# Kernel optimization log

Measured on AMD Instinct MI355X. Metric: run time of the kernel, lower is better.

Reference implementation:

```python
import jax, jax.numpy as jnp
import numpy as np

# ---- config (matches init_kwargs) ----
B, NP, DIM, HEADS, DH, NDIM = 32, 576, 512, 8, 64, 16
N = NP + 1                 # seq len incl cls token = 577
INNER = HEADS * DH         # 512


def setup_inputs() -> dict:
    key = jax.random.key(0)
    ks = jax.random.split(key, 11)
    D2 = 2 * DIM  # bidirectional EMA doubles kernel dim
    return {
        "x": jax.random.normal(ks[0], (B, N, DIM), jnp.float32),
        "W_qk": jax.random.normal(ks[1], (DIM, 2 * INNER), jnp.float32) / np.float32(np.sqrt(DIM)),
        "W_v": jax.random.normal(ks[2], (DIM, INNER), jnp.float32) / np.float32(np.sqrt(DIM)),
        "W_out": jax.random.normal(ks[3], (INNER, DIM), jnp.float32) / np.float32(np.sqrt(INNER)),
        "b_out": jnp.zeros((DIM,), jnp.float32),
        "rel_bias": jax.random.normal(ks[4], (2 * N - 1,), jnp.float32) * 0.02,
        "ema_delta": jax.random.normal(ks[5], (D2, NDIM, 1), jnp.float32),
        "ema_alpha": jax.random.normal(ks[6], (D2, NDIM, 1), jnp.float32),
        "ema_beta": jax.random.normal(ks[7], (D2, NDIM, 1), jnp.float32) * 0.5,
        "ema_gamma": jax.random.normal(ks[8], (D2, NDIM), jnp.float32) * 0.5,
        "ema_omega": jax.random.normal(ks[9], (DIM,), jnp.float32),
    }


def _ema_move(x, delta, alpha, beta, gamma, omega):
    """Bidirectional MultiHeadEMA (MEGA) via FFT convolution. x: (B, L, D)."""
    b, L, d = x.shape
    scale = jnp.asarray(np.sqrt(1.0 / NDIM), x.dtype)
    p = jax.nn.sigmoid(delta)                      # (2D, N, 1)
    q = 1.0 - p * jax.nn.sigmoid(alpha)            # (2D, N, 1), in (0,1)
    vander = jnp.arange(L, dtype=x.dtype)[None, None, :] * jnp.log(q)  # (2D, N, L)
    kern = (p * beta) * jnp.exp(vander)            # (2D, N, L)
    k = jnp.einsum('dnl,dn->dl', kern, gamma * scale)  # (2D, L)
    k1, k2 = k[:d], k[d:]
    # combined bidirectional kernel, length 2L-1
    kk = jnp.pad(k1, ((0, 0), (L - 1, 0))) + jnp.pad(k2[:, ::-1], ((0, 0), (0, L - 1)))
    xt = jnp.pad(x.transpose(0, 2, 1), ((0, 0), (0, 0), (L - 1, 0)))  # (B, D, 2L-1)
    fft_len = 2 * L - 1
    nfft = 2 * fft_len
    out = jnp.fft.irfft(jnp.fft.rfft(xt, n=nfft) * jnp.fft.rfft(kk, n=nfft)[None], n=nfft)
    s = 2 * L - 2
    out = out[..., s:s + L].transpose(0, 2, 1).astype(x.dtype)  # (B, L, D)
    return jax.nn.silu(out + x * omega)


def _rel_pos_bias(rb, seq_len):
    """RelativePositionalBias (MEGA): (2*N-1,) param -> (seq_len, seq_len) bias."""
    max_pos = N
    bvec = rb[max_pos - seq_len: max_pos + seq_len - 1]   # (2*seq_len-1,)
    t = jnp.pad(bvec, (0, seq_len))
    t = jnp.tile(t, seq_len)[:-seq_len].reshape(seq_len, 3 * seq_len - 2)
    r = (2 * seq_len - 1) // 2
    return t[:, r:t.shape[1] - r]


def reference(x, W_qk, W_v, W_out, b_out, rel_bias,
              ema_delta, ema_alpha, ema_beta, ema_gamma, ema_omega):
    b, n, _ = x.shape
    cls_tok = x[:, :1]
    moved = _ema_move(x[:, 1:], ema_delta, ema_alpha, ema_beta, ema_gamma, ema_omega)
    xm = jnp.concatenate([cls_tok, moved], axis=1)        # (B, N, DIM)
    q, k = jnp.split(xm @ W_qk, 2, axis=-1)
    v = xm @ W_v                                          # smooth_v_as_well=True

    def heads(t):
        return t.reshape(b, n, HEADS, DH).transpose(0, 2, 1, 3)  # (B, H, N, DH)

    q, k, v = heads(q), heads(k), heads(v)
    dots = jnp.einsum('bhid,bhjd->bhij', q, k) * (DH ** -0.5)
    attn = jax.nn.softmax(dots, axis=-1)
    attn = attn + _rel_pos_bias(rel_bias, n)[None, None]  # bias added AFTER softmax
    out = jnp.einsum('bhij,bhjd->bhid', attn, v)
    out = out.transpose(0, 2, 1, 3).reshape(b, n, INNER)
    return out @ W_out + b_out
```

## Files before the change

### kernel.cpp

```cpp
#include <hip/hip_runtime.h>

typedef unsigned short ushort;

typedef __bf16 bf16x8 __attribute__((ext_vector_type(8)));
typedef float  f32x4  __attribute__((ext_vector_type(4)));
typedef float  f32x2  __attribute__((ext_vector_type(2)));
typedef unsigned short u16x8 __attribute__((ext_vector_type(8)));
typedef unsigned short u16x4 __attribute__((ext_vector_type(4)));
typedef unsigned int   u32x2 __attribute__((ext_vector_type(2)));

static constexpr int BB   = 32;
static constexpr int NN   = 577;
static constexpr int LL   = 576;
static constexpr int DIMC = 512;
static constexpr int BN   = BB * NN;

static constexpr size_t SZ_WQKVT = 1536ull * 512 * 2;
static constexpr size_t SZ_WOUTT = 512ull * 512 * 2;
static constexpr size_t SZ_QK    = (size_t)BN * 1024 * 2;
static constexpr size_t SZ_V     = (size_t)BN * 512 * 2;
static constexpr size_t SZ_VT    = 256ull * 64 * 640 * 2;
static constexpr size_t OFF_WQKVT = 0;
static constexpr size_t OFF_WOUTT = OFF_WQKVT + SZ_WQKVT;
static constexpr size_t OFF_QTAB  = OFF_WOUTT + SZ_WOUTT;
static constexpr size_t OFF_CTAB  = OFF_QTAB + 65536;
static constexpr size_t OFF_QK    = OFF_CTAB + 65536;
static constexpr size_t OFF_V     = OFF_QK + SZ_QK;
static constexpr size_t OFF_REGION= OFF_V + SZ_V;
static constexpr size_t OFF_XM    = OFF_REGION;
static constexpr size_t OFF_VT    = OFF_REGION;
static constexpr size_t OFF_AO    = OFF_REGION + SZ_VT;
static constexpr size_t OFF_ST    = OFF_AO;
static constexpr size_t WS_NEEDED = OFF_AO + SZ_V;

__device__ __forceinline__ ushort bf16bits(float f) {
  unsigned int u = __builtin_bit_cast(unsigned int, f);
  u = (u + 0x7fffu + ((u >> 16) & 1u)) >> 16;
  return (ushort)u;
}
__device__ __forceinline__ unsigned int bf16pk(float lo, float hi) {
  unsigned int u0 = __builtin_bit_cast(unsigned int, lo);
  unsigned int u1 = __builtin_bit_cast(unsigned int, hi);
  unsigned int a0 = u0 + 0x7fffu + ((u0 >> 16) & 1u);
  unsigned int a1 = u1 + 0x7fffu + ((u1 >> 16) & 1u);
  return __builtin_amdgcn_perm(a1, a0, 0x07060302);
}
__device__ __forceinline__ float sigmoidf_(float z) { return 1.f / (1.f + __expf(-z)); }
__device__ __forceinline__ float siluf(float z)     { return z / (1.f + __expf(-z)); }
__device__ __forceinline__ void gload16(const ushort* g, ushort* l) {
  __builtin_amdgcn_global_load_lds(
      (const __attribute__((address_space(1))) unsigned int*)g,
      (__attribute__((address_space(3))) unsigned int*)l, 16, 0, 0);
}

__global__ __launch_bounds__(256) void k_prep(
    const float* __restrict__ delta, const float* __restrict__ alpha,
    const float* __restrict__ beta,  const float* __restrict__ gamma,
    const float* __restrict__ Wqk,   const float* __restrict__ Wv,
    const float* __restrict__ Wout,
    float* __restrict__ qtab, float* __restrict__ ctab,
    ushort* __restrict__ Wqkvt, ushort* __restrict__ Woutt)
{
  int idx = blockIdx.x * 256 + threadIdx.x;
  if (idx < 16384) {
    float p = sigmoidf_(delta[idx]);
    float q = 1.f - p * sigmoidf_(alpha[idx]);
    qtab[idx] = q;
    ctab[idx] = p * beta[idx] * gamma[idx] * 0.25f;
  }
  int i2 = idx - 16384;
  if (i2 >= 0 && i2 < 1536 * 512) {
    int n = i2 >> 9, k = i2 & 511;
    float w = (n < 1024) ? Wqk[k * 1024 + n] : Wv[k * 512 + (n - 1024)];
    Wqkvt[i2] = bf16bits(w);
  }
  int i3 = i2 - 1536 * 512;
  if (i3 >= 0 && i3 < 512 * 512) {
    int n = i3 >> 9, k = i3 & 511;
    Woutt[i3] = bf16bits(Wout[k * 512 + n]);
  }
}


__global__ __launch_bounds__(64) void k_ema_p1(
    const float* __restrict__ x, const float* __restrict__ qtab,
    float* __restrict__ st)
{
  const int gx = blockIdx.x, cy = blockIdx.y, b = blockIdx.z;
  if (gx < 8) {
    const int d = gx * 64 + threadIdx.x;
    f32x2 q[8], h[8];
    #pragma unroll
    for (int n = 0; n < 8; ++n) {
      q[n] = *(const f32x2*)(qtab + d * 16 + 2 * n);
      h[n] = (f32x2){0.f, 0.f};
    }
    const float* xp = x + ((size_t)b * NN + 1) * DIMC + d;
    const int blo = cy * 9;
    float xn[8];
    #pragma unroll
    for (int u = 0; u < 8; ++u) xn[u] = xp[(blo * 8 + u) * DIMC];
    for (int blk = blo; blk < blo + 9; ++blk) {
      float xv[8];
      #pragma unroll
      for (int u = 0; u < 8; ++u) xv[u] = xn[u];
      if (blk < blo + 8) {
        #pragma unroll
        for (int u = 0; u < 8; ++u) xn[u] = xp[((blk + 1) * 8 + u) * DIMC];
      }
      #pragma unroll
      for (int u = 0; u < 8; ++u) {
        f32x2 x2 = {xv[u], xv[u]};
        #pragma unroll
        for (int n = 0; n < 8; ++n) h[n] = __builtin_elementwise_fma(q[n], h[n], x2);
      }
    }
    float* sp = st + (((size_t)b * 8 + cy) * 16) * 512 + d;
    #pragma unroll
    for (int n = 0; n < 8; ++n) { sp[(2*n) * 512] = h[n][0]; sp[(2*n+1) * 512] = h[n][1]; }
  } else {
    const int d = (gx - 8) * 64 + threadIdx.x;
    f32x2 q[8], g[8];
    #pragma unroll
    for (int n = 0; n < 8; ++n) {
      q[n] = *(const f32x2*)(qtab + (d + 512) * 16 + 2 * n);
      g[n] = (f32x2){0.f, 0.f};
    }
    const float* xp = x + ((size_t)b * NN + 1) * DIMC + d;
    const int blo = (7 - cy) * 9;
    float xn[8];
    #pragma unroll
    for (int u = 0; u < 8; ++u) xn[u] = xp[((blo + 8) * 8 + u) * DIMC];
    for (int blk = blo + 8; blk >= blo; --blk) {
      float xv[8];
      #pragma unroll
      for (int u = 0; u < 8; ++u) xv[u] = xn[u];
      if (blk > blo) {
        #pragma unroll
        for (int u = 0; u < 8; ++u) xn[u] = xp[((blk - 1) * 8 + u) * DIMC];
      }
      #pragma unroll
      for (int u = 7; u >= 0; --u) {
        f32x2 x2 = {xv[u], xv[u]};
        #pragma unroll
        for (int n = 0; n < 8; ++n) g[n] = __builtin_elementwise_fma(q[n], g[n], x2);
      }
    }
    float* sp = st + (((size_t)(32 + b) * 8 + cy) * 16) * 512 + d;
    #pragma unroll
    for (int n = 0; n < 8; ++n) { sp[(2*n) * 512] = g[n][0]; sp[(2*n+1) * 512] = g[n][1]; }
  }
}

__global__ __launch_bounds__(256) void k_ema_mid(
    const float* __restrict__ qtab, float* __restrict__ st)
{
  int idx = blockIdx.x * 256 + threadIdx.x;
  int d = idx & 511;
  int rest = idx >> 9;
  int n = rest & 15;
  int db = rest >> 4;
  int dir = db >> 5;
  float q = qtab[(((size_t)dir << 9) + d) * 16 + n];
  float q2 = q * q, q4 = q2 * q2, q8 = q4 * q4;
  float q16 = q8 * q8, q32 = q16 * q16, q64 = q32 * q32;
  float qL = q64 * q8;
  float h = 0.f;
  float* sp = st + ((size_t)db * 128 + n) * 512 + d;
  #pragma unroll
  for (int c = 0; c < 8; ++c) {
    float tmp = (c < 7) ? sp[c * 8192] : 0.f;
    sp[c * 8192] = h;
    h = fmaf(qL, h, tmp);
  }
}

__global__ __launch_bounds__(64) void k_ema_fuse(
    const float* __restrict__ x, const float* __restrict__ qtab,
    const float* __restrict__ ctab, const float* __restrict__ st,
    const float* __restrict__ omega, ushort* __restrict__ xm)
{
  __shared__ _Float16 yb[72 * 64];
  const int lane = threadIdx.x;
  const int gx = blockIdx.x, cy = blockIdx.y, b = blockIdx.z;
  const int d = gx * 64 + lane;
  const float* xp = x + ((size_t)b * NN + 1 + cy * 72) * DIMC + d;
  {
    f32x2 q[8], c[8], g[8];
    const float* sp = st + (((size_t)(32 + b) * 8 + (7 - cy)) * 16) * 512 + d;
    #pragma unroll
    for (int n = 0; n < 8; ++n) {
      q[n] = *(const f32x2*)(qtab + (d + 512) * 16 + 2 * n);
      c[n] = *(const f32x2*)(ctab + (d + 512) * 16 + 2 * n);
      g[n] = (f32x2){sp[(2*n) * 512], sp[(2*n+1) * 512]};
    }
    float xn[8];
    #pragma unroll
    for (int u = 0; u < 8; ++u) xn[u] = xp[(64 + u) * DIMC];
    for (int blk = 8; blk >= 0; --blk) {
      float xv[8];
      #pragma unroll
      for (int u = 0; u < 8; ++u) xv[u] = xn[u];
      if (blk > 0) {
        #pragma unroll
        for (int u = 0; u < 8; ++u) xn[u] = xp[((blk - 1) * 8 + u) * DIMC];
      }
      #pragma unroll
      for (int u = 7; u >= 0; --u) {
        f32x2 x2 = {xv[u], xv[u]};
        f32x2 yv = {0.f, 0.f};
        #pragma unroll
        for (int n = 0; n < 8; ++n) {
          g[n] = __builtin_elementwise_fma(q[n], g[n], x2);
          yv   = __builtin_elementwise_fma(c[n], g[n], yv);
        }
        yb[(blk * 8 + u) * 64 + lane] = (_Float16)(yv[0] + yv[1]);
      }
    }
  }
  __syncthreads();
  {
    f32x2 q[8], c[8], h[8];
    const float* sp = st + (((size_t)b * 8 + cy) * 16) * 512 + d;
    #pragma unroll
    for (int n = 0; n < 8; ++n) {
      q[n] = *(const f32x2*)(qtab + d * 16 + 2 * n);
      c[n] = *(const f32x2*)(ctab + d * 16 + 2 * n);
      h[n] = (f32x2){sp[(2*n) * 512], sp[(2*n+1) * 512]};
    }
    const float om = omega[d];
    ushort* op = xm + ((size_t)b * NN + 1 + cy * 72) * DIMC + d;
    float xn[8];
    #pragma unroll
    for (int u = 0; u < 8; ++u) xn[u] = xp[u * DIMC];
    for (int blk = 0; blk < 9; ++blk) {
      float xv[8];
      #pragma unroll
      for (int u = 0; u < 8; ++u) xv[u] = xn[u];
      if (blk < 8) {
        #pragma unroll
        for (int u = 0; u < 8; ++u) xn[u] = xp[((blk + 1) * 8 + u) * DIMC];
      }
      #pragma unroll
      for (int u = 0; u < 8; ++u) {
        f32x2 x2 = {xv[u], xv[u]};
        f32x2 yv = {0.f, 0.f};
        #pragma unroll
        for (int n = 0; n < 8; ++n) {
          h[n] = __builtin_elementwise_fma(q[n], h[n], x2);
          yv   = __builtin_elementwise_fma(c[n], h[n], yv);
        }
        float s = (yv[0] + yv[1]) + (float)yb[(blk * 8 + u) * 64 + lane] + xv[u] * om;
        op[(blk * 8 + u) * DIMC] = bf16bits(siluf(s));
      }
    }
  }
  if (cy == 0) {
    size_t e0 = ((size_t)b * NN) * DIMC + d;
    xm[e0] = bf16bits(x[e0]);
  }
}

__global__ __launch_bounds__(256) void k_qkv(
    const ushort* __restrict__ A, const ushort* __restrict__ Bt,
    ushort* __restrict__ qk, ushort* __restrict__ v)
{
  __shared__ alignas(16) ushort lA[128 * 32];
  __shared__ alignas(16) ushort lB[128 * 32];
  const int tid = threadIdx.x, wv = tid >> 6, lane = tid & 63;
  const int quad = lane >> 4, c16 = lane & 15;
  const int fid = blockIdx.y * 12 + blockIdx.x;
  const int xcd = fid & 7, ord = fid >> 3;
  const int wg  = (xcd < 4 ? xcd * 218 : 872 + (xcd - 4) * 217) + ord;
  const int row0 = (wg / 12) * 128, n0 = (wg % 12) * 128;
  const int wm = (wv >> 1) * 64, wn = (wv & 1) * 64;
  const int sr  = wv * 32 + (lane >> 2);
  const int scs = ((lane & 3) ^ (sr & 3)) * 8;
  int ga[2], gb[2];
  #pragma unroll
  for (int s = 0; s < 2; ++s) {
    int r = row0 + sr + s * 16; if (r > BN - 1) r = BN - 1;
    ga[s] = r;
    gb[s] = n0 + sr + s * 16;
  }
  const int xread = (quad ^ (c16 & 3)) * 8;
  f32x4 z4 = {0.f, 0.f, 0.f, 0.f};
  f32x4 acc[4][4];
  #pragma unroll
  for (int mi = 0; mi < 4; ++mi)
    #pragma unroll
    for (int ni = 0; ni < 4; ++ni) acc[mi][ni] = z4;

  for (int kt = 0; kt < 16; ++kt) {
    const int k0 = kt * 32;
    __syncthreads();
    #pragma unroll
    for (int s = 0; s < 2; ++s) {
      gload16(A  + (size_t)ga[s] * 512 + k0 + scs, lA + (wv * 32 + s * 16) * 32);
      gload16(Bt + (size_t)gb[s] * 512 + k0 + scs, lB + (wv * 32 + s * 16) * 32);
    }
    __syncthreads();
    bf16x8 af[4], bfv[4];
    #pragma unroll
    for (int mi = 0; mi < 4; ++mi)
      af[mi] = *(const bf16x8*)(lA + (wm + mi * 16 + c16) * 32 + xread);
    #pragma unroll
    for (int ni = 0; ni < 4; ++ni)
      bfv[ni] = *(const bf16x8*)(lB + (wn + ni * 16 + c16) * 32 + xread);
    #pragma unroll
    for (int mi = 0; mi < 4; ++mi)
      #pragma unroll
      for (int ni = 0; ni < 4; ++ni)
        acc[mi][ni] = __builtin_amdgcn_mfma_f32_16x16x32_bf16(af[mi], bfv[ni], acc[mi][ni], 0, 0, 0);
  }
  const bool isv = (n0 >= 1024);
  const float osc = (n0 < 512) ? 0.1803368801111f : 1.0f;
  #pragma unroll
  for (int mi = 0; mi < 4; ++mi) {
    #pragma unroll
    for (int r = 0; r < 4; ++r) {
      int grow = row0 + wm + mi * 16 + quad * 4 + r;
      if (grow < BN) {
        #pragma unroll
        for (int ni = 0; ni < 4; ++ni) {
          int col = n0 + wn + ni * 16 + c16;
          ushort vb = bf16bits(acc[mi][ni][r] * osc);
          if (!isv) qk[(size_t)grow * 1024 + col] = vb;
          else      v[(size_t)grow * 512 + (col - 1024)] = vb;
        }
      }
    }
  }
}

__global__ __launch_bounds__(256) void k_vtrans(
    const ushort* __restrict__ v, ushort* __restrict__ vt)
{
  __shared__ alignas(16) ushort lt[64 * 72];
  const int tid = threadIdx.x;
  const int bh = blockIdx.y, b = bh >> 3, h = bh & 7;
  const int j0 = blockIdx.x * 64;
  #pragma unroll
  for (int pass = 0; pass < 2; ++pass) {
    int cch = pass * 256 + tid;
    int jl = cch >> 3, cc = cch & 7;
    int gj = j0 + jl;
    u16x8 val = {0, 0, 0, 0, 0, 0, 0, 0};
    if (gj < 577) val = *(const u16x8*)(v + ((size_t)(b * NN + gj)) * 512 + h * 64 + cc * 8);
    *(u16x8*)(lt + jl * 72 + cc * 8) = val;
  }
  __syncthreads();
  #pragma unroll
  for (int pass = 0; pass < 2; ++pass) {
    int cch = pass * 256 + tid;
    int dh = cch >> 3, jc = cch & 7;
    u16x8 o;
    #pragma unroll
    for (int e = 0; e < 8; ++e) o[e] = lt[(jc * 8 + e) * 72 + dh];
    *(u16x8*)(vt + ((size_t)(bh * 64 + dh)) * 640 + j0 + jc * 8) = o;
  }
}

__global__ __launch_bounds__(256) void k_fattn(
    const ushort* __restrict__ qk, const ushort* __restrict__ vt,
    const float* __restrict__ relb, ushort* __restrict__ ao)
{
  __shared__ alignas(16) ushort lk[64 * 64];
  __shared__ alignas(16) ushort lv[64 * 64];
  __shared__ alignas(16) ushort lp[64 * 64];
  __shared__ ushort lbias16[1280];
  const int tid = threadIdx.x, wv = tid >> 6, lane = tid & 63;
  const int quad = lane >> 4, c16 = lane & 15;
  const int bh = blockIdx.x, b = bh >> 3, h = bh & 7;
  const int i0 = blockIdx.y * 64, wm = wv * 16;
  for (int t = tid; t < 1280; t += 256) {
    int idx = t - 64;
    lbias16[t] = (idx >= 0 && idx < 1153) ? bf16bits(relb[idx]) : (ushort)0;
  }
  bf16x8 aq[2];
  {
    int gi = i0 + wm + c16; if (gi > 576) gi = 576;
    const ushort* qp = qk + ((size_t)(b * NN + gi)) * 1024 + h * 64;
    #pragma unroll
    for (int kk = 0; kk < 2; ++kk)
      aq[kk] = *(const bf16x8*)(qp + (kk * 4 + quad) * 8);
  }
  const int s_r = tid >> 3, s_c = tid & 7;
  const ushort* kbase = qk + ((size_t)b * NN) * 1024 + 512 + h * 64 + s_c * 8;
  const ushort* vbase = vt + ((size_t)bh * 64) * 640 + s_c * 8;

  float lsum = 0.f;
  f32x4 z4 = {0.f, 0.f, 0.f, 0.f};
  f32x4 accp[4], accb[4];
  #pragma unroll
  for (int ns = 0; ns < 4; ++ns) { accp[ns] = z4; accb[ns] = z4; }

  u16x8 sk[2], sv[2];
  #pragma unroll
  for (int it = 0; it < 2; ++it) {
    int r = it * 32 + s_r;
    sk[it] = *(const u16x8*)(kbase + (size_t)r * 1024);
    sv[it] = *(const u16x8*)(vbase + (size_t)r * 640);
  }

  for (int jt = 0; jt < 10; ++jt) {
    __syncthreads();
    #pragma unroll
    for (int it = 0; it < 2; ++it) {
      int r = it * 32 + s_r;
      int pc = (s_c ^ (r & 7)) * 8;
      *(u16x8*)(lk + r * 64 + pc) = sk[it];
      *(u16x8*)(lv + r * 64 + pc) = sv[it];
    }
    __syncthreads();
    if (jt < 9) {
      const int j0n = (jt + 1) * 64;
      #pragma unroll
      for (int it = 0; it < 2; ++it) {
        int r = it * 32 + s_r;
        int gj = j0n + r; if (gj > 576) gj = 576;
        sk[it] = *(const u16x8*)(kbase + (size_t)gj * 1024);
        sv[it] = *(const u16x8*)(vbase + (size_t)r * 640 + j0n);
      }
    }
    f32x4 dacc[4] = {z4, z4, z4, z4};
    #pragma unroll
    for (int kk = 0; kk < 2; ++kk) {
      const int ck = kk * 4 + quad;
      #pragma unroll
      for (int ns = 0; ns < 4; ++ns) {
        const int row = ns * 16 + c16;
        bf16x8 bk = *(const bf16x8*)(lk + row * 64 + ((ck ^ (row & 7)) * 8));
        dacc[ns] = __builtin_amdgcn_mfma_f32_16x16x32_bf16(bk, aq[kk], dacc[ns], 0, 0, 0);
      }
    }
    {
      const int irow = wm + c16;
      const int xr = irow & 7;
      #pragma unroll
      for (int ns = 0; ns < 4; ++ns) {
        float ex[4];
        #pragma unroll
        for (int r = 0; r < 4; ++r) {
          float e = __builtin_amdgcn_exp2f(dacc[ns][r]);
          if (jt == 9 && (ns * 16 + quad * 4 + r) >= 1) e = 0.f;
          ex[r] = e;
        }
        lsum += (ex[0] + ex[1]) + (ex[2] + ex[3]);
        u32x2 pw = { bf16pk(ex[0], ex[1]), bf16pk(ex[2], ex[3]) };
        const int lc = ns * 2 + (quad >> 1);
        *(u32x2*)(lp + irow * 64 + ((lc ^ xr) * 8) + (quad & 1) * 4) = pw;
      }
    }
    const int j0 = jt * 64;
    #pragma unroll
    for (int kk = 0; kk < 2; ++kk) {
      const int ck = kk * 4 + quad;
      const int row = wm + c16;
      bf16x8 ap = *(const bf16x8*)(lp + row * 64 + ((ck ^ (row & 7)) * 8));
      u16x8 abu;
      const int base = 64 + 576 + j0 + kk * 32 + quad * 8 - (i0 + row);
      #pragma unroll
      for (int e = 0; e < 8; ++e) abu[e] = lbias16[base + e];
      bf16x8 ab = __builtin_bit_cast(bf16x8, abu);
      #pragma unroll
      for (int ns = 0; ns < 4; ++ns) {
        const int vrow = ns * 16 + c16;
        bf16x8 bV = *(const bf16x8*)(lv + vrow * 64 + ((ck ^ (vrow & 7)) * 8));
        accp[ns] = __builtin_amdgcn_mfma_f32_16x16x32_bf16(ap, bV, accp[ns], 0, 0, 0);
        accb[ns] = __builtin_amdgcn_mfma_f32_16x16x32_bf16(ab, bV, accb[ns], 0, 0, 0);
      }
    }
  }
  float tot = lsum;
  tot += __shfl_xor(tot, 16);
  tot += __shfl_xor(tot, 32);
  #pragma unroll
  for (int r = 0; r < 4; ++r) {
    float li = 1.f / __shfl(tot, quad * 4 + r);
    int ii = i0 + wm + quad * 4 + r;
    if (ii < 577) {
      #pragma unroll
      for (int ns = 0; ns < 4; ++ns)
        ao[((size_t)(b * NN + ii)) * 512 + h * 64 + ns * 16 + c16] =
            bf16bits(accp[ns][r] * li + accb[ns][r]);
    }
  }
}

__global__ __launch_bounds__(256) void k_out(
    const ushort* __restrict__ A, const ushort* __restrict__ Bt,
    const float* __restrict__ bout, float* __restrict__ out)
{
  __shared__ alignas(16) ushort lA[128 * 32];
  __shared__ alignas(16) ushort lB[128 * 32];
  const int tid = threadIdx.x, wv = tid >> 6, lane = tid & 63;
  const int quad = lane >> 4, c16 = lane & 15;
  const int row0 = blockIdx.y * 128, n0 = blockIdx.x * 128;
  const int wm = (wv >> 1) * 64, wn = (wv & 1) * 64;
  const int sr  = wv * 32 + (lane >> 2);
  const int scs = ((lane & 3) ^ (sr & 3)) * 8;
  int ga[2], gb[2];
  #pragma unroll
  for (int s = 0; s < 2; ++s) {
    int r = row0 + sr + s * 16; if (r > BN - 1) r = BN - 1;
    ga[s] = r;
    gb[s] = n0 + sr + s * 16;
  }
  const int xread = (quad ^ (c16 & 3)) * 8;
  f32x4 z4 = {0.f, 0.f, 0.f, 0.f};
  f32x4 acc[4][4];
  #pragma unroll
  for (int mi = 0; mi < 4; ++mi)
    #pragma unroll
    for (int ni = 0; ni < 4; ++ni) acc[mi][ni] = z4;

  for (int kt = 0; kt < 16; ++kt) {
    const int k0 = kt * 32;
    __syncthreads();
    #pragma unroll
    for (int s = 0; s < 2; ++s) {
      gload16(A  + (size_t)ga[s] * 512 + k0 + scs, lA + (wv * 32 + s * 16) * 32);
      gload16(Bt + (size_t)gb[s] * 512 + k0 + scs, lB + (wv * 32 + s * 16) * 32);
    }
    __syncthreads();
    bf16x8 af[4], bfv[4];
    #pragma unroll
    for (int mi = 0; mi < 4; ++mi)
      af[mi] = *(const bf16x8*)(lA + (wm + mi * 16 + c16) * 32 + xread);
    #pragma unroll
    for (int ni = 0; ni < 4; ++ni)
      bfv[ni] = *(const bf16x8*)(lB + (wn + ni * 16 + c16) * 32 + xread);
    #pragma unroll
    for (int mi = 0; mi < 4; ++mi)
      #pragma unroll
      for (int ni = 0; ni < 4; ++ni)
        acc[mi][ni] = __builtin_amdgcn_mfma_f32_16x16x32_bf16(af[mi], bfv[ni], acc[mi][ni], 0, 0, 0);
  }
  #pragma unroll
  for (int mi = 0; mi < 4; ++mi) {
    #pragma unroll
    for (int r = 0; r < 4; ++r) {
      int grow = row0 + wm + mi * 16 + quad * 4 + r;
      if (grow < BN) {
        #pragma unroll
        for (int ni = 0; ni < 4; ++ni) {
          int col = n0 + wn + ni * 16 + c16;
          out[(size_t)grow * 512 + col] = acc[mi][ni][r] + bout[col];
        }
      }
    }
  }
}

extern "C" void kernel_launch(void* const* d_in, const int* in_sizes, int n_in,
                              void* d_out, int out_size, void* d_ws, size_t ws_size,
                              hipStream_t stream) {
  (void)in_sizes; (void)n_in; (void)out_size;
  if (ws_size < WS_NEEDED) return;
  const float* x    = (const float*)d_in[0];
  const float* Wqk  = (const float*)d_in[1];
  const float* Wv   = (const float*)d_in[2];
  const float* Wout = (const float*)d_in[3];
  const float* bout = (const float*)d_in[4];
  const float* relb = (const float*)d_in[5];
  const float* edel = (const float*)d_in[6];
  const float* ealp = (const float*)d_in[7];
  const float* ebet = (const float*)d_in[8];
  const float* egam = (const float*)d_in[9];
  const float* eome = (const float*)d_in[10];

  char* ws = (char*)d_ws;
  ushort* Wqkvt = (ushort*)(ws + OFF_WQKVT);
  ushort* Woutt = (ushort*)(ws + OFF_WOUTT);
  float*  qtab  = (float*)(ws + OFF_QTAB);
  float*  ctab  = (float*)(ws + OFF_CTAB);
  ushort* qkb   = (ushort*)(ws + OFF_QK);
  ushort* vb    = (ushort*)(ws + OFF_V);
  ushort* xm    = (ushort*)(ws + OFF_XM);
  ushort* vtb   = (ushort*)(ws + OFF_VT);
  ushort* aob   = (ushort*)(ws + OFF_AO);
  float*  stf   = (float*)(ws + OFF_ST);
  float*  outp  = (float*)d_out;

  k_prep<<<dim3(4160), dim3(256), 0, stream>>>(edel, ealp, ebet, egam, Wqk, Wv, Wout,
                                               qtab, ctab, Wqkvt, Woutt);
  k_ema_p1<<<dim3(16, 7, 32), dim3(64), 0, stream>>>(x, qtab, stf);
  k_ema_mid<<<dim3(2048), dim3(256), 0, stream>>>(qtab, stf);
  k_ema_fuse<<<dim3(8, 8, 32), dim3(64), 0, stream>>>(x, qtab, ctab, stf, eome, xm);
  k_qkv<<<dim3(12, 145), dim3(256), 0, stream>>>(xm, Wqkvt, qkb, vb);
  k_vtrans<<<dim3(10, 256), dim3(256), 0, stream>>>(vb, vtb);
  k_fattn<<<dim3(256, 10), dim3(256), 0, stream>>>(qkb, vtb, relb, aob);
  k_out<<<dim3(4, 145), dim3(256), 0, stream>>>(aob, Woutt, bout, outp);
}
```

Measured before the change: 307.6 us.

## Double-buffer K/V tiles with direct global-to-LDS loads and 128-row query tiles

The attention kernel now uses two LDS buffers for K and V. The next tile is loaded with gload16 (direct global-to-LDS copies) while the current one is computed, which removes one barrier per iteration and the register staging. Each block now handles 128 query rows (two 16-row sub-tiles per wave), so every K/V tile loaded is reused twice and the grid shrinks to half. In exchange it uses more LDS and registers and launches fewer blocks, which can lower occupancy. The last tile now pads 128 rows instead of 64.

Result: faster. 296.9 us (-3.5%).

```diff
diff --git a/kernel.cpp b/kernel.cpp
--- a/kernel.cpp
+++ b/kernel.cpp
@@ -365,77 +365,76 @@
     const ushort* __restrict__ qk, const ushort* __restrict__ vt,
     const float* __restrict__ relb, ushort* __restrict__ ao)
 {
-  __shared__ alignas(16) ushort lk[64 * 64];
-  __shared__ alignas(16) ushort lv[64 * 64];
-  __shared__ alignas(16) ushort lp[64 * 64];
+  __shared__ alignas(16) ushort lk0[64 * 64];
+  __shared__ alignas(16) ushort lk1[64 * 64];
+  __shared__ alignas(16) ushort lv0[64 * 64];
+  __shared__ alignas(16) ushort lv1[64 * 64];
+  __shared__ alignas(16) ushort lp[128 * 64];
   __shared__ ushort lbias16[1280];
   const int tid = threadIdx.x, wv = tid >> 6, lane = tid & 63;
   const int quad = lane >> 4, c16 = lane & 15;
   const int bh = blockIdx.x, b = bh >> 3, h = bh & 7;
-  const int i0 = blockIdx.y * 64, wm = wv * 16;
+  const int i0 = blockIdx.y * 128, wm = wv * 32;
   for (int t = tid; t < 1280; t += 256) {
     int idx = t - 64;
     lbias16[t] = (idx >= 0 && idx < 1153) ? bf16bits(relb[idx]) : (ushort)0;
   }
-  bf16x8 aq[2];
-  {
-    int gi = i0 + wm + c16; if (gi > 576) gi = 576;
+  bf16x8 aq[2][2];
+  #pragma unroll
+  for (int ms = 0; ms < 2; ++ms) {
+    int gi = i0 + wm + ms * 16 + c16; if (gi > 576) gi = 576;
     const ushort* qp = qk + ((size_t)(b * NN + gi)) * 1024 + h * 64;
     #pragma unroll
     for (int kk = 0; kk < 2; ++kk)
-      aq[kk] = *(const bf16x8*)(qp + (kk * 4 + quad) * 8);
-  }
-  const int s_r = tid >> 3, s_c = tid & 7;
-  const ushort* kbase = qk + ((size_t)b * NN) * 1024 + 512 + h * 64 + s_c * 8;
-  const ushort* vbase = vt + ((size_t)bh * 64) * 640 + s_c * 8;
-
-  float lsum = 0.f;
+      aq[ms][kk] = *(const bf16x8*)(qp + (kk * 4 + quad) * 8);
+  }
+  const int lr = lane >> 3, lc = lane & 7;
+  const ushort* kroot = qk + ((size_t)b * NN) * 1024 + 512 + h * 64;
+  const ushort* vroot = vt + ((size_t)bh * 64) * 640;
+
+  float lsum[2] = {0.f, 0.f};
   f32x4 z4 = {0.f, 0.f, 0.f, 0.f};
-  f32x4 accp[4], accb[4];
-  #pragma unroll
-  for (int ns = 0; ns < 4; ++ns) { accp[ns] = z4; accb[ns] = z4; }
-
-  u16x8 sk[2], sv[2];
-  #pragma unroll
-  for (int it = 0; it < 2; ++it) {
-    int r = it * 32 + s_r;
-    sk[it] = *(const u16x8*)(kbase + (size_t)r * 1024);
-    sv[it] = *(const u16x8*)(vbase + (size_t)r * 640);
-  }
+  f32x4 accp[2][4], accb[2][4];
+  #pragma unroll
+  for (int ms = 0; ms < 2; ++ms)
+    #pragma unroll
+    for (int ns = 0; ns < 4; ++ns) { accp[ms][ns] = z4; accb[ms][ns] = z4; }
+
+  #define STAGE_TILE(J0, DK, DV)                                              \
+    {                                                                         \
+      _Pragma("unroll")                                                       \
+      for (int s = 0; s < 2; ++s) {                                           \
+        const int r  = wv * 16 + s * 8 + lr;                                  \
+        const int sc = (lc ^ (r & 7)) * 8;                                    \
+        int gj = (J0) + r; if (gj > 576) gj = 576;                            \
+        gload16(kroot + (size_t)gj * 1024 + sc, (DK) + (wv * 16 + s * 8) * 64); \
+        gload16(vroot + (size_t)r * 640 + (J0) + sc, (DV) + (wv * 16 + s * 8) * 64); \
+      }                                                                       \
+    }
+
+  STAGE_TILE(0, lk0, lv0)
 
   for (int jt = 0; jt < 10; ++jt) {
+    const ushort* ck_ = (jt & 1) ? lk1 : lk0;
+    const ushort* cv_ = (jt & 1) ? lv1 : lv0;
+    ushort* nk_ = (jt & 1) ? lk0 : lk1;
+    ushort* nv_ = (jt & 1) ? lv0 : lv1;
     __syncthreads();
-    #pragma unroll
-    for (int it = 0; it < 2; ++it) {
-      int r = it * 32 + s_r;
-      int pc = (s_c ^ (r & 7)) * 8;
-      *(u16x8*)(lk + r * 64 + pc) = sk[it];
-      *(u16x8*)(lv + r * 64 + pc) = sv[it];
-    }
-    __syncthreads();
-    if (jt < 9) {
-      const int j0n = (jt + 1) * 64;
-      #pragma unroll
-      for (int it = 0; it < 2; ++it) {
-        int r = it * 32 + s_r;
-        int gj = j0n + r; if (gj > 576) gj = 576;
-        sk[it] = *(const u16x8*)(kbase + (size_t)gj * 1024);
-        sv[it] = *(const u16x8*)(vbase + (size_t)r * 640 + j0n);
-      }
-    }
-    f32x4 dacc[4] = {z4, z4, z4, z4};
-    #pragma unroll
-    for (int kk = 0; kk < 2; ++kk) {
-      const int ck = kk * 4 + quad;
-      #pragma unroll
-      for (int ns = 0; ns < 4; ++ns) {
-        const int row = ns * 16 + c16;
-        bf16x8 bk = *(const bf16x8*)(lk + row * 64 + ((ck ^ (row & 7)) * 8));
-        dacc[ns] = __builtin_amdgcn_mfma_f32_16x16x32_bf16(bk, aq[kk], dacc[ns], 0, 0, 0);
-      }
-    }
-    {
-      const int irow = wm + c16;
+    if (jt < 9) STAGE_TILE((jt + 1) * 64, nk_, nv_)
+    #pragma unroll
+    for (int ms = 0; ms < 2; ++ms) {
+      f32x4 dacc[4] = {z4, z4, z4, z4};
+      #pragma unroll
+      for (int kk = 0; kk < 2; ++kk) {
+        const int ck = kk * 4 + quad;
+        #pragma unroll
+        for (int ns = 0; ns < 4; ++ns) {
+          const int row = ns * 16 + c16;
+          bf16x8 bk = *(const bf16x8*)(ck_ + row * 64 + ((ck ^ (row & 7)) * 8));
+          dacc[ns] = __builtin_amdgcn_mfma_f32_16x16x32_bf16(bk, aq[ms][kk], dacc[ns], 0, 0, 0);
+        }
+      }
+      const int irow = wm + ms * 16 + c16;
       const int xr = irow & 7;
       #pragma unroll
       for (int ns = 0; ns < 4; ++ns) {
@@ -446,44 +445,60 @@
           if (jt == 9 && (ns * 16 + quad * 4 + r) >= 1) e = 0.f;
           ex[r] = e;
         }
-        lsum += (ex[0] + ex[1]) + (ex[2] + ex[3]);
+        lsum[ms] += (ex[0] + ex[1]) + (ex[2] + ex[3]);
         u32x2 pw = { bf16pk(ex[0], ex[1]), bf16pk(ex[2], ex[3]) };
-        const int lc = ns * 2 + (quad >> 1);
-        *(u32x2*)(lp + irow * 64 + ((lc ^ xr) * 8) + (quad & 1) * 4) = pw;
+        const int lc2 = ns * 2 + (quad >> 1);
+        *(u32x2*)(lp + irow * 64 + ((lc2 ^ xr) * 8) + (quad & 1) * 4) = pw;
       }
     }
     const int j0 = jt * 64;
     #pragma unroll
     for (int kk = 0; kk < 2; ++kk) {
       const int ck = kk * 4 + quad;
-      const int row = wm + c16;
-      bf16x8 ap = *(const bf16x8*)(lp + row * 64 + ((ck ^ (row & 7)) * 8));
-      u16x8 abu;
-      const int base = 64 + 576 + j0 + kk * 32 + quad * 8 - (i0 + row);
-      #pragma unroll
-      for (int e = 0; e < 8; ++e) abu[e] = lbias16[base + e];
-      bf16x8 ab = __builtin_bit_cast(bf16x8, abu);
+      bf16x8 ap[2], ab[2];
+      #pragma unroll
+      for (int ms = 0; ms < 2; ++ms) {
+        const int row = wm + ms * 16 + c16;
+        ap[ms] = *(const bf16x8*)(lp + row * 64 + ((ck ^ (row & 7)) * 8));
+        u16x8 abu;
+        const int base = 64 + 576 + j0 + kk * 32 + quad * 8 - (i0 + row);
+        #pragma unroll
+        for (int e = 0; e < 8; ++e) abu[e] = lbias16[base + e];
+        ab[ms] = __builtin_bit_cast(bf16x8, abu);
+      }
       #pragma unroll
       for (int ns = 0; ns < 4; ++ns) {
-        const int vrow = ns * 16 + c16;
-        bf16x8 bV = *(const bf16x8*)(lv + vrow * 64 + ((ck ^ (vrow & 7)) * 8));
-        accp[ns] = __builtin_amdgcn_mfma_f32_16x16x32_bf16(ap, bV, accp[ns], 0, 0, 0);
-        accb[ns] = __builtin_amdgcn_mfma_f32_16x16x32_bf16(ab, bV, accb[ns], 0, 0, 0);
-      }
-    }
-  }
-  float tot = lsum;
-  tot += __shfl_xor(tot, 16);
-  tot += __shfl_xor(tot, 32);
-  #pragma unroll
-  for (int r = 0; r < 4; ++r) {
-    float li = 1.f / __shfl(tot, quad * 4 + r);
-    int ii = i0 + wm + quad * 4 + r;
-    if (ii < 577) {
-      #pragma unroll
-      for (int ns = 0; ns < 4; ++ns)
-        ao[((size_t)(b * NN + ii)) * 512 + h * 64 + ns * 16 + c16] =
-            bf16bits(accp[ns][r] * li + accb[ns][r]);
+        const int row = ns * 16 + c16;
+        bf16x8 bV = *(const bf16x8*)(cv_ + row * 64 + ((ck ^ (row & 7)) * 8));
+        #pragma unroll
+        for (int ms = 0; ms < 2; ++ms) {
+          accp[ms][ns] = __builtin_amdgcn_mfma_f32_16x16x32_bf16(ap[ms], bV, accp[ms][ns], 0, 0, 0);
+          accb[ms][ns] = __builtin_amdgcn_mfma_f32_16x16x32_bf16(ab[ms], bV, accb[ms][ns], 0, 0, 0);
+        }
+      }
+    }
+  }
+  #undef STAGE_TILE
+  float tot[2];
+  #pragma unroll
+  for (int ms = 0; ms < 2; ++ms) {
+    float t = lsum[ms];
+    t += __shfl_xor(t, 16);
+    t += __shfl_xor(t, 32);
+    tot[ms] = t;
+  }
+  #pragma unroll
+  for (int ms = 0; ms < 2; ++ms) {
+    #pragma unroll
+    for (int r = 0; r < 4; ++r) {
+      float li = 1.f / __shfl(tot[ms], quad * 4 + r);
+      int ii = i0 + wm + ms * 16 + quad * 4 + r;
+      if (ii < 577) {
+        #pragma unroll
+        for (int ns = 0; ns < 4; ++ns)
+          ao[((size_t)(b * NN + ii)) * 512 + h * 64 + ns * 16 + c16] =
+              bf16bits(accp[ms][ns][r] * li + accb[ms][ns][r]);
+      }
     }
   }
 }
@@ -590,6 +605,6 @@
   k_ema_fuse<<<dim3(8, 8, 32), dim3(64), 0, stream>>>(x, qtab, ctab, stf, eome, xm);
   k_qkv<<<dim3(12, 145), dim3(256), 0, stream>>>(xm, Wqkvt, qkb, vb);
   k_vtrans<<<dim3(10, 256), dim3(256), 0, stream>>>(vb, vtb);
-  k_fattn<<<dim3(256, 10), dim3(256), 0, stream>>>(qkb, vtb, relb, aob);
+  k_fattn<<<dim3(256, 5), dim3(256), 0, stream>>>(qkb, vtb, relb, aob);
   k_out<<<dim3(4, 145), dim3(256), 0, stream>>>(aob, Woutt, bout, outp);
 }
```

## Stage QKV GEMM epilogue through LDS and double query tile per attention block

Applied to the files above, without the earlier changes.

The QKV GEMM epilogue now writes its accumulators into shared memory and stores them as coalesced 16-byte rows, replacing scattered 2-byte stores. The attention kernel moves to 512 threads and 128 query rows per block, so each K/V tile loaded into LDS serves twice as many queries. This halves the number of attention blocks and their redundant K/V traffic. The cost is more LDS per block, fewer blocks to spread across CUs (1280 instead of 2560), and extra barriers in the GEMM epilogue.

Result: faster. 294.4 us (-4.3%).

```diff
diff --git a/kernel.cpp b/kernel.cpp
--- a/kernel.cpp
+++ b/kernel.cpp
@@ -265,8 +265,9 @@
     const ushort* __restrict__ A, const ushort* __restrict__ Bt,
     ushort* __restrict__ qk, ushort* __restrict__ v)
 {
-  __shared__ alignas(16) ushort lA[128 * 32];
-  __shared__ alignas(16) ushort lB[128 * 32];
+  __shared__ alignas(16) ushort lsh[8192];
+  ushort* lA = lsh;
+  ushort* lB = lsh + 4096;
   const int tid = threadIdx.x, wv = tid >> 6, lane = tid & 63;
   const int quad = lane >> 4, c16 = lane & 15;
   const int fid = blockIdx.y * 12 + blockIdx.x;
@@ -316,18 +317,29 @@
   const bool isv = (n0 >= 1024);
   const float osc = (n0 < 512) ? 0.1803368801111f : 1.0f;
   #pragma unroll
-  for (int mi = 0; mi < 4; ++mi) {
-    #pragma unroll
-    for (int r = 0; r < 4; ++r) {
-      int grow = row0 + wm + mi * 16 + quad * 4 + r;
+  for (int hh = 0; hh < 2; ++hh) {
+    __syncthreads();
+    if ((wv >> 1) == hh) {
+      #pragma unroll
+      for (int mi = 0; mi < 4; ++mi)
+        #pragma unroll
+        for (int r = 0; r < 4; ++r) {
+          int lrow = mi * 16 + quad * 4 + r;
+          #pragma unroll
+          for (int ni = 0; ni < 4; ++ni)
+            lsh[lrow * 128 + wn + ni * 16 + c16] = bf16bits(acc[mi][ni][r] * osc);
+        }
+    }
+    __syncthreads();
+    #pragma unroll
+    for (int pass = 0; pass < 4; ++pass) {
+      int lrow = pass * 16 + (tid >> 4);
+      int cc = (tid & 15) * 8;
+      int grow = row0 + hh * 64 + lrow;
       if (grow < BN) {
-        #pragma unroll
-        for (int ni = 0; ni < 4; ++ni) {
-          int col = n0 + wn + ni * 16 + c16;
-          ushort vb = bf16bits(acc[mi][ni][r] * osc);
-          if (!isv) qk[(size_t)grow * 1024 + col] = vb;
-          else      v[(size_t)grow * 512 + (col - 1024)] = vb;
-        }
+        u16x8 val = *(const u16x8*)(lsh + lrow * 128 + cc);
+        if (!isv) *(u16x8*)(qk + (size_t)grow * 1024 + n0 + cc) = val;
+        else      *(u16x8*)(v  + (size_t)grow * 512 + (n0 - 1024) + cc) = val;
       }
     }
   }
@@ -361,19 +373,19 @@
   }
 }
 
-__global__ __launch_bounds__(256) void k_fattn(
+__global__ __launch_bounds__(512) void k_fattn(
     const ushort* __restrict__ qk, const ushort* __restrict__ vt,
     const float* __restrict__ relb, ushort* __restrict__ ao)
 {
   __shared__ alignas(16) ushort lk[64 * 64];
   __shared__ alignas(16) ushort lv[64 * 64];
-  __shared__ alignas(16) ushort lp[64 * 64];
+  __shared__ alignas(16) ushort lp[128 * 64];
   __shared__ ushort lbias16[1280];
   const int tid = threadIdx.x, wv = tid >> 6, lane = tid & 63;
   const int quad = lane >> 4, c16 = lane & 15;
   const int bh = blockIdx.x, b = bh >> 3, h = bh & 7;
-  const int i0 = blockIdx.y * 64, wm = wv * 16;
-  for (int t = tid; t < 1280; t += 256) {
+  const int i0 = blockIdx.y * 128, wm = wv * 16;
+  for (int t = tid; t < 1280; t += 512) {
     int idx = t - 64;
     lbias16[t] = (idx >= 0 && idx < 1153) ? bf16bits(relb[idx]) : (ushort)0;
   }
@@ -395,33 +407,23 @@
   #pragma unroll
   for (int ns = 0; ns < 4; ++ns) { accp[ns] = z4; accb[ns] = z4; }
 
-  u16x8 sk[2], sv[2];
-  #pragma unroll
-  for (int it = 0; it < 2; ++it) {
-    int r = it * 32 + s_r;
-    sk[it] = *(const u16x8*)(kbase + (size_t)r * 1024);
-    sv[it] = *(const u16x8*)(vbase + (size_t)r * 640);
-  }
+  u16x8 sk, sv;
+  sk = *(const u16x8*)(kbase + (size_t)s_r * 1024);
+  sv = *(const u16x8*)(vbase + (size_t)s_r * 640);
 
   for (int jt = 0; jt < 10; ++jt) {
     __syncthreads();
-    #pragma unroll
-    for (int it = 0; it < 2; ++it) {
-      int r = it * 32 + s_r;
-      int pc = (s_c ^ (r & 7)) * 8;
-      *(u16x8*)(lk + r * 64 + pc) = sk[it];
-      *(u16x8*)(lv + r * 64 + pc) = sv[it];
+    {
+      int pc = (s_c ^ (s_r & 7)) * 8;
+      *(u16x8*)(lk + s_r * 64 + pc) = sk;
+      *(u16x8*)(lv + s_r * 64 + pc) = sv;
     }
     __syncthreads();
     if (jt < 9) {
       const int j0n = (jt + 1) * 64;
-      #pragma unroll
-      for (int it = 0; it < 2; ++it) {
-        int r = it * 32 + s_r;
-        int gj = j0n + r; if (gj > 576) gj = 576;
-        sk[it] = *(const u16x8*)(kbase + (size_t)gj * 1024);
-        sv[it] = *(const u16x8*)(vbase + (size_t)r * 640 + j0n);
-      }
+      int gj = j0n + s_r; if (gj > 576) gj = 576;
+      sk = *(const u16x8*)(kbase + (size_t)gj * 1024);
+      sv = *(const u16x8*)(vbase + (size_t)s_r * 640 + j0n);
     }
     f32x4 dacc[4] = {z4, z4, z4, z4};
     #pragma unroll
@@ -448,8 +450,8 @@
         }
         lsum += (ex[0] + ex[1]) + (ex[2] + ex[3]);
         u32x2 pw = { bf16pk(ex[0], ex[1]), bf16pk(ex[2], ex[3]) };
-        const int lc = ns * 2 + (quad >> 1);
-        *(u32x2*)(lp + irow * 64 + ((lc ^ xr) * 8) + (quad & 1) * 4) = pw;
+        const int lc2 = ns * 2 + (quad >> 1);
+        *(u32x2*)(lp + irow * 64 + ((lc2 ^ xr) * 8) + (quad & 1) * 4) = pw;
       }
     }
     const int j0 = jt * 64;
@@ -590,6 +592,6 @@
   k_ema_fuse<<<dim3(8, 8, 32), dim3(64), 0, stream>>>(x, qtab, ctab, stf, eome, xm);
   k_qkv<<<dim3(12, 145), dim3(256), 0, stream>>>(xm, Wqkvt, qkb, vb);
   k_vtrans<<<dim3(10, 256), dim3(256), 0, stream>>>(vb, vtb);
-  k_fattn<<<dim3(256, 10), dim3(256), 0, stream>>>(qkb, vtb, relb, aob);
+  k_fattn<<<dim3(256, 5), dim3(512), 0, stream>>>(qkb, vtb, relb, aob);
   k_out<<<dim3(4, 145), dim3(256), 0, stream>>>(aob, Woutt, bout, outp);
 }
```
